# Kernel tuning notes

Measured on AMD Instinct MI355X. Metric: run time of the kernel, lower is better.

The kernel has to match this reference:

```python
import jax, jax.numpy as jnp
import numpy as np


def setup_inputs() -> dict:
    key = jax.random.key(0)
    ks = jax.random.split(key, 6)
    B, C, H, W = 8, 512, 64, 64
    s = 1.0 / np.sqrt(C)
    return {
        "x": jax.random.normal(ks[0], (B, C, H, W), dtype=jnp.float32),
        "w_phi": jax.random.normal(ks[1], (C, C), dtype=jnp.float32) * s,
        "w_theta": jax.random.normal(ks[2], (C, C), dtype=jnp.float32) * s,
        "w_g": jax.random.normal(ks[3], (C, C), dtype=jnp.float32) * s,
        "w_mask": jax.random.normal(ks[4], (C, C), dtype=jnp.float32) * s,
        "gamma": jax.random.normal(ks[5], (1,), dtype=jnp.float32) * 0.1,
    }


def reference(x, w_phi, w_theta, w_g, w_mask, gamma):
    b, c, h, w = x.shape
    n = h * w
    xf = x.reshape(b, c, n)  # flatten spatial: [b, c, n]
    # 1x1 convs (bias=False) are channel-mixing GEMMs
    phi = jnp.einsum("oc,bcn->bon", w_phi, xf)    # [b, c, n]
    theta = jnp.einsum("oc,bcn->bon", w_theta, xf)  # [b, c, n]
    g = jnp.einsum("oc,bcn->bon", w_g, xf)        # [b, c, n]
    # channel-channel attention (unscaled), softmax over last dim
    attn = jax.nn.softmax(jnp.einsum("bcn,bdn->bcd", phi, theta), axis=-1)  # [b, c, c]
    y = jnp.einsum("bcd,bdn->bcn", attn, g)  # [b, c, n]
    # faithful to torch: permute(0,2,1).contiguous().view(b, c, h, w)
    y = jnp.transpose(y, (0, 2, 1)).reshape(b, c, h, w)
    mask = jnp.einsum("oc,bchw->bohw", w_mask, y)
    return mask * gamma[0] + x
```

## Files before the change

### kernel.cpp

```cpp
#include <hip/hip_runtime.h>
#include <hip/hip_bf16.h>

constexpr int BATCH = 8;
constexpr int C = 512;
constexpr int HW = 4096;
constexpr long CN = (long)C * HW;
constexpr long CC = (long)C * C;

typedef __attribute__((ext_vector_type(8))) short short8;
typedef __attribute__((ext_vector_type(4))) short bf16x4;
typedef __attribute__((ext_vector_type(4))) float f32x4;

__device__ __forceinline__ void gload16(const void* g, void* l) {
  __builtin_amdgcn_global_load_lds(
      (const __attribute__((address_space(1))) void*)g,
      (__attribute__((address_space(3))) void*)l, 16, 0, 0);
}

__device__ __forceinline__ void hilo(float v, __hip_bfloat16& h, __hip_bfloat16& l) {
  h = __float2bfloat16(v);
  l = __float2bfloat16(v - __bfloat162float(h));
}
__device__ __forceinline__ short bfs(float v) {
  __hip_bfloat16 h = __float2bfloat16(v);
  return *(short*)&h;
}

__device__ __forceinline__ int cidx32(int r, int ch) {
  return ((r >> 1) * 8 + ((((r & 1) << 2) | ch) ^ ((r >> 1) & 7))) * 8;
}
__device__ __forceinline__ void sdec32(int s, int& r, int& ch) {
  int R = s >> 3, q = s & 7, v = q ^ (R & 7);
  r = (R << 1) | (v >> 2);
  ch = v & 3;
}

#define WAIT_VM(n) asm volatile("s_waitcnt vmcnt(" #n ")" ::: "memory")

__global__ __launch_bounds__(256) void convx_k(
    const float* __restrict__ x, __hip_bfloat16* __restrict__ xhi,
    __hip_bfloat16* __restrict__ xt) {
  const int b = blockIdx.z;
  const int n0 = blockIdx.x * 64, c0 = blockIdx.y * 64;
  const float* xb = x + (long)b * CN;
  __shared__ short t[64 * 65];
  const int tid = threadIdx.x;
#pragma unroll
  for (int it = 0; it < 2; ++it) {
    int slot = it * 256 + tid;
    int r = slot >> 3, cc = (slot & 7) * 8;
    const float* src = xb + (long)(c0 + r) * HW + n0 + cc;
    f32x4 v0 = *(const f32x4*)src, v1 = *(const f32x4*)(src + 4);
    short8 hh;
#pragma unroll
    for (int e = 0; e < 4; ++e) {
      hh[e] = bfs(v0[e]);
      hh[4 + e] = bfs(v1[e]);
    }
    long idx = (long)b * CN + (long)(c0 + r) * HW + n0 + cc;
    *(short8*)((short*)xhi + idx) = hh;
#pragma unroll
    for (int e = 0; e < 8; ++e) t[r * 65 + cc + e] = hh[e];
  }
  __syncthreads();
#pragma unroll
  for (int it = 0; it < 2; ++it) {
    int slot = it * 256 + tid;
    int r = slot >> 3, cc = (slot & 7) * 8;
    short8 o;
#pragma unroll
    for (int e = 0; e < 8; ++e) o[e] = t[(cc + e) * 65 + r];
    *(short8*)((short*)xt + (long)b * CN + (long)(n0 + r) * C + c0 + cc) = o;
  }
}

__global__ __launch_bounds__(256) void wprep_k(
    const float* __restrict__ wphi, const float* __restrict__ wtheta,
    const float* __restrict__ wg, const float* __restrict__ wmask,
    __hip_bfloat16* __restrict__ wph, __hip_bfloat16* __restrict__ wpl,
    __hip_bfloat16* __restrict__ wth, __hip_bfloat16* __restrict__ wtl,
    __hip_bfloat16* __restrict__ wgT, __hip_bfloat16* __restrict__ wm16) {
  const int z = blockIdx.z;
  const int r0 = blockIdx.y * 64, c0 = blockIdx.x * 64;
  const int tid = threadIdx.x;
  if (z == 2) {
    __shared__ __hip_bfloat16 t[64][65];
#pragma unroll
    for (int i = 0; i < 16; ++i) {
      int e = i * 256 + tid;
      int r = e >> 6, c = e & 63;
      t[r][c] = __float2bfloat16(wg[(long)(r0 + r) * C + c0 + c]);
    }
    __syncthreads();
#pragma unroll
    for (int i = 0; i < 16; ++i) {
      int e = i * 256 + tid;
      int r = e >> 6, c = e & 63;
      wgT[(long)(c0 + r) * C + r0 + c] = t[c][r];
    }
  } else {
#pragma unroll
    for (int i = 0; i < 16; ++i) {
      int e = i * 256 + tid;
      int r = e >> 6, c = e & 63;
      long idx = (long)(r0 + r) * C + c0 + c;
      if (z == 0) {
        __hip_bfloat16 h, l;
        hilo(wphi[idx], h, l);
        wph[idx] = h; wpl[idx] = l;
      } else if (z == 1) {
        __hip_bfloat16 h, l;
        hilo(wtheta[idx], h, l);
        wth[idx] = h; wtl[idx] = l;
      } else {
        wm16[idx] = __float2bfloat16(wmask[idx]);
      }
    }
  }
}

__global__ __launch_bounds__(256) void gram_k(
    const __hip_bfloat16* __restrict__ xhi, float* __restrict__ gpart) {
  const int f = blockIdx.x + 10 * (blockIdx.y + 4 * blockIdx.z);
  const int b = f & 7;
  const int rdec = f >> 3;
  const int ks = rdec / 10;
  const int tile = rdec % 10;
  int i = 0, rem0 = tile;
  while (rem0 >= 4 - i) { rem0 -= 4 - i; ++i; }
  const int j = i + rem0;
  const int m0 = i * 128, n0 = j * 128;

  const short* X = (const short*)(xhi + (long)b * CN);
  __shared__ short lds[4 * 8192];
  const int tid = threadIdx.x, w = tid >> 6, lane = tid & 63;

  f32x4 acc[4][4] = {};
  const int wr = (w >> 1) * 64, wc = (w & 1) * 64;
  const int kbeg = ks * 1024;
  constexpr int NST = 32;

  auto STAGE = [&](int buf, int k0) {
#pragma unroll
    for (int it = 0; it < 4; ++it) {
      int s = (w & 1) * 256 + it * 64 + lane;
      int r, ch;
      sdec32(s, r, ch);
      int gr = (w < 2) ? (m0 + r) : (n0 + r);
      gload16(X + (long)gr * HW + k0 + ch * 8, lds + (buf * 8192 + (w >> 1) * 4096 + s * 8));
    }
  };

  const int chf = lane >> 4, rl = lane & 15;
  int aoff[4], boff[4];
#pragma unroll
  for (int mi = 0; mi < 4; ++mi) aoff[mi] = cidx32(wr + mi * 16 + rl, chf);
#pragma unroll
  for (int ni = 0; ni < 4; ++ni) boff[ni] = 4096 + cidx32(wc + ni * 16 + rl, chf);

  STAGE(0, kbeg);
  STAGE(1, kbeg + 32);
  STAGE(2, kbeg + 64);

#pragma unroll
  for (int t = 0; t < NST; ++t) {
    if (t + 3 < NST) STAGE((t + 3) & 3, kbeg + (t + 3) * 32);
    const int rm = NST - 1 - t;
    if (rm >= 3) WAIT_VM(12);
    else if (rm == 2) WAIT_VM(8);
    else if (rm == 1) WAIT_VM(4);
    else WAIT_VM(0);
    __builtin_amdgcn_s_barrier();
    const short* lb = lds + (t & 3) * 8192;
    short8 af[4], bfr[4];
#pragma unroll
    for (int mi = 0; mi < 4; ++mi) af[mi] = *(const short8*)(lb + aoff[mi]);
#pragma unroll
    for (int ni = 0; ni < 4; ++ni) bfr[ni] = *(const short8*)(lb + boff[ni]);
#pragma unroll
    for (int mi = 0; mi < 4; ++mi)
#pragma unroll
      for (int ni = 0; ni < 4; ++ni)
        acc[mi][ni] = __builtin_amdgcn_mfma_f32_16x16x32_bf16(af[mi], bfr[ni], acc[mi][ni], 0, 0, 0);
    __builtin_amdgcn_s_barrier();
  }

  float* P = gpart + ((((long)b * 10 + tile) * 4 + ks) << 14);
#pragma unroll
  for (int mi = 0; mi < 4; ++mi)
#pragma unroll
    for (int ni = 0; ni < 4; ++ni)
#pragma unroll
      for (int rr = 0; rr < 4; ++rr) {
        int row = wr + mi * 16 + (lane >> 4) * 4 + rr;
        int col = wc + ni * 16 + (lane & 15);
        P[row * 128 + col] = acc[mi][ni][rr];
      }
}

__global__ __launch_bounds__(256) void gred_k(
    const float* __restrict__ gpart, __hip_bfloat16* __restrict__ gh,
    __hip_bfloat16* __restrict__ gl) {
  const int id = blockIdx.x;
  const int b = id & 7;
  const int t2 = id >> 3;
  const int tile = t2 % 10;
  const int half = t2 / 10;
  int i = 0, rem = tile;
  while (rem >= 4 - i) { rem -= 4 - i; ++i; }
  const int j = i + rem;
  const int m0 = i * 128, n0 = j * 128;
  const float* P = gpart + (((long)b * 10 + tile) << 16) + half * 8192;
  __shared__ float T[128][65];
  const int tid = threadIdx.x;
  const long dbase = (long)b * CC;

#pragma unroll
  for (int q = 0; q < 8; ++q) {
    int e = q * 1024 + tid * 4;
    int r = e >> 7, c = e & 127;
    f32x4 s = {};
#pragma unroll
    for (int ks = 0; ks < 4; ++ks) s += *(const f32x4*)(P + (ks << 14) + e);
    bf16x4 hh, ll;
#pragma unroll
    for (int u = 0; u < 4; ++u) {
      __hip_bfloat16 h, l;
      hilo(s[u], h, l);
      hh[u] = *(short*)&h;
      ll[u] = *(short*)&l;
      T[c + u][r] = s[u];
    }
    long idx = dbase + (long)(m0 + half * 64 + r) * 512 + n0 + c;
    *(bf16x4*)((short*)gh + idx) = hh;
    *(bf16x4*)((short*)gl + idx) = ll;
  }
  if (i != j) {
    __syncthreads();
#pragma unroll
    for (int q = 0; q < 8; ++q) {
      int e = q * 1024 + tid * 4;
      int rp = e >> 6, cp = e & 63;
      bf16x4 hh, ll;
#pragma unroll
      for (int u = 0; u < 4; ++u) {
        __hip_bfloat16 h, l;
        hilo(T[rp][cp + u], h, l);
        hh[u] = *(short*)&h;
        ll[u] = *(short*)&l;
      }
      long idx = dbase + (long)(n0 + rp) * 512 + m0 + half * 64 + cp;
      *(bf16x4*)((short*)gh + idx) = hh;
      *(bf16x4*)((short*)gl + idx) = ll;
    }
  }
}

template <int AH, int BH, int EPI>
__global__ __launch_bounds__(256) void nt_small(
    const __hip_bfloat16* __restrict__ Ah_, const __hip_bfloat16* __restrict__ Al_,
    const __hip_bfloat16* __restrict__ Bh_, const __hip_bfloat16* __restrict__ Bl_,
    long aStr, long bStr, void* __restrict__ out1, void* __restrict__ out2) {
  const int id = blockIdx.x;
  const int b = id & 7;
  const int rest = id >> 3;
  const int m0 = (rest >> 3) * 64, n0 = (rest & 7) * 64;
  const short* Ahp = (const short*)(Ah_ + (long)b * aStr);
  const short* Alp = AH ? (const short*)(Al_ + (long)b * aStr) : nullptr;
  const short* Bhp = (const short*)(Bh_ + (long)b * bStr);
  const short* Blp = BH ? (const short*)(Bl_ + (long)b * bStr) : nullptr;
  constexpr int PAN = (AH && BH) ? 4 : 2;
  __shared__ short lds[2 * PAN * 4096];
  const int tid = threadIdx.x, w = tid >> 6, lane = tid & 63;

  f32x4 acc[2][2] = {};
  const int wr = (w >> 1) * 32, wc = (w & 1) * 32;

  auto STAGE = [&](int buf, int k0) {
    short* lb = lds + buf * PAN * 4096;
    if constexpr (AH && BH) {
      const short* src = (w == 0) ? Ahp : (w == 1) ? Alp : (w == 2) ? Bhp : Blp;
      const int rowbase = (w & 2) ? n0 : m0;
      short* lt = lb + w * 4096;
#pragma unroll
      for (int it = 0; it < 8; ++it) {
        int slot = it * 64 + lane;
        int r = slot >> 3, p = slot & 7, c = p ^ (r & 7);
        gload16(src + (long)(rowbase + r) * 512 + k0 + c * 8, lt + slot * 8);
      }
    } else {
      const short* src = (w < 2) ? Ahp : Bhp;
      const int rowbase = (w < 2) ? m0 : n0;
      short* lt = lb + (w >> 1) * 4096;
#pragma unroll
      for (int it = 0; it < 4; ++it) {
        int slot = (w & 1) * 256 + it * 64 + lane;
        int r = slot >> 3, p = slot & 7, c = p ^ (r & 7);
        gload16(src + (long)(rowbase + r) * 512 + k0 + c * 8, lt + slot * 8);
      }
    }
  };

  STAGE(0, 0);
  asm volatile("s_waitcnt vmcnt(0)" ::: "memory");
  __builtin_amdgcn_s_barrier();

  for (int t = 0; t < 8; ++t) {
    if (t < 7) STAGE((t + 1) & 1, (t + 1) * 64);
    const short* lb = lds + (t & 1) * PAN * 4096;
#pragma unroll
    for (int kh = 0; kh < 2; ++kh) {
      short8 ah[2], al[2], bh[2], bl[2];
      const int ch = kh * 4 + (lane >> 4);
#pragma unroll
      for (int mi = 0; mi < 2; ++mi) {
        int r = wr + mi * 16 + (lane & 15);
        int off = (r * 8 + (ch ^ (r & 7))) * 8;
        ah[mi] = *(const short8*)(lb + off);
        if constexpr (AH) al[mi] = *(const short8*)(lb + 4096 + off);
      }
#pragma unroll
      for (int ni = 0; ni < 2; ++ni) {
        int r = wc + ni * 16 + (lane & 15);
        int off = (r * 8 + (ch ^ (r & 7))) * 8;
        bh[ni] = *(const short8*)(lb + ((AH && BH) ? 8192 : 4096) + off);
        if constexpr (BH) bl[ni] = *(const short8*)(lb + 12288 + off);
      }
#pragma unroll
      for (int mi = 0; mi < 2; ++mi)
#pragma unroll
        for (int ni = 0; ni < 2; ++ni) {
          acc[mi][ni] = __builtin_amdgcn_mfma_f32_16x16x32_bf16(ah[mi], bh[ni], acc[mi][ni], 0, 0, 0);
          if constexpr (BH)
            acc[mi][ni] = __builtin_amdgcn_mfma_f32_16x16x32_bf16(ah[mi], bl[ni], acc[mi][ni], 0, 0, 0);
          if constexpr (AH)
            acc[mi][ni] = __builtin_amdgcn_mfma_f32_16x16x32_bf16(al[mi], bh[ni], acc[mi][ni], 0, 0, 0);
        }
    }
    asm volatile("s_waitcnt vmcnt(0)" ::: "memory");
    __builtin_amdgcn_s_barrier();
  }

#pragma unroll
  for (int mi = 0; mi < 2; ++mi)
#pragma unroll
    for (int ni = 0; ni < 2; ++ni)
#pragma unroll
      for (int rr = 0; rr < 4; ++rr) {
        int row = m0 + wr + mi * 16 + (lane >> 4) * 4 + rr;
        int col = n0 + wc + ni * 16 + (lane & 15);
        long idx = (long)b * CC + (long)row * 512 + col;
        float v = acc[mi][ni][rr];
        if constexpr (EPI == 0) {
          __hip_bfloat16 h, l;
          hilo(v, h, l);
          ((__hip_bfloat16*)out1)[idx] = h;
          ((__hip_bfloat16*)out2)[idx] = l;
        } else if constexpr (EPI == 1) {
          ((float*)out1)[idx] = v;
        } else {
          ((__hip_bfloat16*)out1)[idx] = __float2bfloat16(v);
        }
      }
}

__global__ __launch_bounds__(256) void softmax_k(const float* __restrict__ a,
                                                 __hip_bfloat16* __restrict__ o) {
  const int id = blockIdx.x;
  const int b = id & 7, rg = id >> 3;
  const int w = threadIdx.x >> 6, lane = threadIdx.x & 63;
  const long row = (long)b * 512 + rg * 4 + w;
  const float* rp = a + row * 512 + lane * 8;
  f32x4 v0 = *(const f32x4*)rp, v1 = *(const f32x4*)(rp + 4);
  float mx = fmaxf(fmaxf(fmaxf(v0[0], v0[1]), fmaxf(v0[2], v0[3])),
                   fmaxf(fmaxf(v1[0], v1[1]), fmaxf(v1[2], v1[3])));
#pragma unroll
  for (int s = 1; s < 64; s <<= 1) mx = fmaxf(mx, __shfl_xor(mx, s));
  float e[8];
#pragma unroll
  for (int k = 0; k < 4; ++k) {
    e[k] = expf(v0[k] - mx);
    e[4 + k] = expf(v1[k] - mx);
  }
  float sum = ((e[0] + e[1]) + (e[2] + e[3])) + ((e[4] + e[5]) + (e[6] + e[7]));
#pragma unroll
  for (int s = 1; s < 64; s <<= 1) sum += __shfl_xor(sum, s);
  const float inv = 1.0f / sum;
  short8 o8;
#pragma unroll
  for (int k = 0; k < 8; ++k) o8[k] = bfs(e[k] * inv);
  *(short8*)((short*)o + row * 512 + lane * 8) = o8;
}

template <int MODE>
__global__ __launch_bounds__(256) void big_k(
    const __hip_bfloat16* __restrict__ Aw, const __hip_bfloat16* __restrict__ Bm,
    void* __restrict__ Cout, const float* __restrict__ x,
    const float* __restrict__ gammaPtr, long aStride) {
  const int b = blockIdx.z;
  const int lin = ((blockIdx.x & 7) << 4) | (blockIdx.x >> 3);
  const int m0 = (lin & 3) * 128;
  const int n0 = (lin >> 2) * 128;
  const short* A = (const short*)(Aw + (long)b * aStride);
  const short* B = (const short*)(Bm + (long)b * CN);
  __shared__ short lds[4 * 8192];
  const int tid = threadIdx.x, w = tid >> 6, lane = tid & 63;

  f32x4 acc[4][4] = {};
  const int wr = (w >> 1) * 64, wc = (w & 1) * 64;
  constexpr int NST = 16;

  auto STAGE = [&](int buf, int k0) {
    short* lb = lds + buf * 8192;
#pragma unroll
    for (int it = 0; it < 4; ++it) {
      int s = (w & 1) * 256 + it * 64 + lane;
      int r, ch;
      sdec32(s, r, ch);
      if (w < 2) {
        gload16(A + (long)(m0 + r) * 512 + k0 + ch * 8, lb + s * 8);
      } else {
        int gr = (MODE == 0) ? (n0 + (r & 15) * 8 + (r >> 4)) : (n0 + r);
        gload16(B + (long)gr * 512 + k0 + ch * 8, lb + 4096 + s * 8);
      }
    }
  };

  const int chf = lane >> 4, rl = lane & 15;
  int aoff[4], boff[4];
#pragma unroll
  for (int mi = 0; mi < 4; ++mi) aoff[mi] = cidx32(wr + mi * 16 + rl, chf);
#pragma unroll
  for (int ni = 0; ni < 4; ++ni) boff[ni] = 4096 + cidx32(wc + ni * 16 + rl, chf);

  STAGE(0, 0);
  STAGE(1, 32);
  STAGE(2, 64);

#pragma unroll
  for (int t = 0; t < NST; ++t) {
    if (t + 3 < NST) STAGE((t + 3) & 3, (t + 3) * 32);
    const int rm = NST - 1 - t;
    if (rm >= 3) WAIT_VM(12);
    else if (rm == 2) WAIT_VM(8);
    else if (rm == 1) WAIT_VM(4);
    else WAIT_VM(0);
    __builtin_amdgcn_s_barrier();
    const short* lb = lds + (t & 3) * 8192;
    short8 af[4], bfr[4];
#pragma unroll
    for (int mi = 0; mi < 4; ++mi) af[mi] = *(const short8*)(lb + aoff[mi]);
#pragma unroll
    for (int ni = 0; ni < 4; ++ni) bfr[ni] = *(const short8*)(lb + boff[ni]);
#pragma unroll
    for (int mi = 0; mi < 4; ++mi)
#pragma unroll
      for (int ni = 0; ni < 4; ++ni)
        acc[mi][ni] = __builtin_amdgcn_mfma_f32_16x16x32_bf16(af[mi], bfr[ni], acc[mi][ni], 0, 0, 0);
    __builtin_amdgcn_s_barrier();
  }

  if (MODE == 0) {
    __hip_bfloat16* yv = (__hip_bfloat16*)Cout + (long)b * CN;
    const int u = lane & 15;
#pragma unroll
    for (int mi = 0; mi < 4; ++mi)
#pragma unroll
      for (int ni = 0; ni < 4; ++ni) {
        int t = (wc >> 4) + ni;
        long base = ((long)(t * 512 + m0 + wr + mi * 16 + (lane >> 4) * 4)) * 512 +
                    (n0 >> 3) + u;
#pragma unroll
        for (int r = 0; r < 4; ++r)
          yv[base + (long)r * 512] = __float2bfloat16(acc[mi][ni][r]);
      }
  } else {
    float* outp = (float*)Cout + (long)b * CN;
    const float* xb = x + (long)b * CN;
    const float g0 = gammaPtr[0];
#pragma unroll
    for (int mi = 0; mi < 4; ++mi)
#pragma unroll
      for (int ni = 0; ni < 4; ++ni)
#pragma unroll
        for (int r = 0; r < 4; ++r) {
          long idx = (long)(m0 + wr + mi * 16 + (lane >> 4) * 4 + r) * HW +
                     n0 + wc + ni * 16 + (lane & 15);
          outp[idx] = g0 * acc[mi][ni][r] + xb[idx];
        }
  }
}

extern "C" void kernel_launch(void* const* d_in, const int* in_sizes, int n_in,
                              void* d_out, int out_size, void* d_ws, size_t ws_size,
                              hipStream_t stream) {
  const float* x       = (const float*)d_in[0];
  const float* w_phi   = (const float*)d_in[1];
  const float* w_theta = (const float*)d_in[2];
  const float* w_g     = (const float*)d_in[3];
  const float* w_mask  = (const float*)d_in[4];
  const float* gamma   = (const float*)d_in[5];
  float* out = (float*)d_out;

  __hip_bfloat16* xhi = (__hip_bfloat16*)d_ws;
  __hip_bfloat16* xt  = xhi + BATCH * CN;
  __hip_bfloat16* gh  = xt + BATCH * CN;
  __hip_bfloat16* gl  = gh + BATCH * CC;
  __hip_bfloat16* t1h = gl + BATCH * CC;
  __hip_bfloat16* t1l = t1h + BATCH * CC;
  __hip_bfloat16* wph = t1l + BATCH * CC;
  __hip_bfloat16* wpl = wph + CC;
  __hip_bfloat16* wth = wpl + CC;
  __hip_bfloat16* wtl = wth + CC;
  __hip_bfloat16* wgT = wtl + CC;
  __hip_bfloat16* wm16 = wgT + CC;
  float* gpart = (float*)(wm16 + CC);
  float* logits           = (float*)gh;
  __hip_bfloat16* attn16  = t1h;
  __hip_bfloat16* mb16    = t1l;
  __hip_bfloat16* yvT     = xhi;

  convx_k<<<dim3(64, 8, BATCH), 256, 0, stream>>>(x, xhi, xt);
  wprep_k<<<dim3(8, 8, 4), 256, 0, stream>>>(w_phi, w_theta, w_g, w_mask,
                                             wph, wpl, wth, wtl, wgT, wm16);
  gram_k<<<dim3(10, 4, BATCH), 256, 0, stream>>>(xhi, gpart);
  gred_k<<<dim3(160, 1, 1), 256, 0, stream>>>(gpart, gh, gl);
  nt_small<1, 1, 0><<<dim3(512, 1, 1), 256, 0, stream>>>(
      wph, wpl, gh, gl, 0, CC, t1h, t1l);
  nt_small<1, 1, 1><<<dim3(512, 1, 1), 256, 0, stream>>>(
      t1h, t1l, wth, wtl, CC, 0, logits, nullptr);
  softmax_k<<<dim3(1024, 1, 1), dim3(256), 0, stream>>>(logits, attn16);
  nt_small<0, 0, 2><<<dim3(512, 1, 1), 256, 0, stream>>>(
      attn16, nullptr, wgT, nullptr, CC, 0, mb16, nullptr);
  big_k<0><<<dim3(128, 1, BATCH), 256, 0, stream>>>(mb16, xt, yvT, nullptr, nullptr, CC);
  big_k<1><<<dim3(128, 1, BATCH), 256, 0, stream>>>(wm16, yvT, out, x, gamma, 0);
}
```

Measured before the change: 255.6 us.

## Deepen nt_small to 4-stage pipeline and prefetch residual x during GEMM loop

The small channel-attention GEMM kernel moves from a double-buffered BK=64 loop with full vmcnt(0) drains to the 4-buffer BK=32 pipeline used by big_k, with partial waitcnts and precomputed swizzled LDS offsets. The final mask GEMM now loads the residual x tile into registers across the K loop, so the epilogue no longer stalls on global reads. The cost is more registers (64 floats of x per thread) in the big kernel, which may lower occupancy. The tuned vmcnt thresholds also have to match the exact number of outstanding loads.

```diff
diff --git a/kernel.cpp b/kernel.cpp
--- a/kernel.cpp
+++ b/kernel.cpp
@@ -270,74 +270,89 @@
   const short* Bhp = (const short*)(Bh_ + (long)b * bStr);
   const short* Blp = BH ? (const short*)(Bl_ + (long)b * bStr) : nullptr;
   constexpr int PAN = (AH && BH) ? 4 : 2;
-  __shared__ short lds[2 * PAN * 4096];
+  constexpr int BUFS = PAN * 2048;
+  __shared__ short lds[4 * BUFS];
   const int tid = threadIdx.x, w = tid >> 6, lane = tid & 63;
 
   f32x4 acc[2][2] = {};
   const int wr = (w >> 1) * 32, wc = (w & 1) * 32;
+  constexpr int NST = 16;
 
   auto STAGE = [&](int buf, int k0) {
-    short* lb = lds + buf * PAN * 4096;
     if constexpr (AH && BH) {
       const short* src = (w == 0) ? Ahp : (w == 1) ? Alp : (w == 2) ? Bhp : Blp;
       const int rowbase = (w & 2) ? n0 : m0;
-      short* lt = lb + w * 4096;
-#pragma unroll
-      for (int it = 0; it < 8; ++it) {
-        int slot = it * 64 + lane;
-        int r = slot >> 3, p = slot & 7, c = p ^ (r & 7);
-        gload16(src + (long)(rowbase + r) * 512 + k0 + c * 8, lt + slot * 8);
+#pragma unroll
+      for (int it = 0; it < 4; ++it) {
+        int s = it * 64 + lane;
+        int r, ch;
+        sdec32(s, r, ch);
+        gload16(src + (long)(rowbase + r) * 512 + k0 + ch * 8,
+                lds + ((buf * PAN + w) * 2048 + s * 8));
       }
     } else {
       const short* src = (w < 2) ? Ahp : Bhp;
       const int rowbase = (w < 2) ? m0 : n0;
-      short* lt = lb + (w >> 1) * 4096;
-#pragma unroll
-      for (int it = 0; it < 4; ++it) {
-        int slot = (w & 1) * 256 + it * 64 + lane;
-        int r = slot >> 3, p = slot & 7, c = p ^ (r & 7);
-        gload16(src + (long)(rowbase + r) * 512 + k0 + c * 8, lt + slot * 8);
+#pragma unroll
+      for (int it = 0; it < 2; ++it) {
+        int s = (w & 1) * 128 + it * 64 + lane;
+        int r, ch;
+        sdec32(s, r, ch);
+        gload16(src + (long)(rowbase + r) * 512 + k0 + ch * 8,
+                lds + ((buf * PAN + (w >> 1)) * 2048 + s * 8));
       }
     }
   };
 
+  const int chf = lane >> 4, rl = lane & 15;
+  int aoff[2], boff[2];
+#pragma unroll
+  for (int mi = 0; mi < 2; ++mi) aoff[mi] = cidx32(wr + mi * 16 + rl, chf);
+#pragma unroll
+  for (int ni = 0; ni < 2; ++ni) boff[ni] = cidx32(wc + ni * 16 + rl, chf);
+
   STAGE(0, 0);
-  asm volatile("s_waitcnt vmcnt(0)" ::: "memory");
-  __builtin_amdgcn_s_barrier();
-
-  for (int t = 0; t < 8; ++t) {
-    if (t < 7) STAGE((t + 1) & 1, (t + 1) * 64);
-    const short* lb = lds + (t & 1) * PAN * 4096;
-#pragma unroll
-    for (int kh = 0; kh < 2; ++kh) {
-      short8 ah[2], al[2], bh[2], bl[2];
-      const int ch = kh * 4 + (lane >> 4);
-#pragma unroll
-      for (int mi = 0; mi < 2; ++mi) {
-        int r = wr + mi * 16 + (lane & 15);
-        int off = (r * 8 + (ch ^ (r & 7))) * 8;
-        ah[mi] = *(const short8*)(lb + off);
-        if constexpr (AH) al[mi] = *(const short8*)(lb + 4096 + off);
-      }
+  STAGE(1, 32);
+  STAGE(2, 64);
+
+#pragma unroll
+  for (int t = 0; t < NST; ++t) {
+    if (t + 3 < NST) STAGE((t + 3) & 3, (t + 3) * 32);
+    const int rm = NST - 1 - t;
+    if constexpr (PAN == 4) {
+      if (rm >= 3) WAIT_VM(12);
+      else if (rm == 2) WAIT_VM(8);
+      else if (rm == 1) WAIT_VM(4);
+      else WAIT_VM(0);
+    } else {
+      if (rm >= 3) WAIT_VM(6);
+      else if (rm == 2) WAIT_VM(4);
+      else if (rm == 1) WAIT_VM(2);
+      else WAIT_VM(0);
+    }
+    __builtin_amdgcn_s_barrier();
+    const short* lb = lds + (t & 3) * BUFS;
+    short8 ah[2], al[2], bh[2], bl[2];
+#pragma unroll
+    for (int mi = 0; mi < 2; ++mi) {
+      ah[mi] = *(const short8*)(lb + aoff[mi]);
+      if constexpr (AH) al[mi] = *(const short8*)(lb + 2048 + aoff[mi]);
+    }
+#pragma unroll
+    for (int ni = 0; ni < 2; ++ni) {
+      bh[ni] = *(const short8*)(lb + ((AH && BH) ? 4096 : 2048) + boff[ni]);
+      if constexpr (BH) bl[ni] = *(const short8*)(lb + 6144 + boff[ni]);
+    }
+#pragma unroll
+    for (int mi = 0; mi < 2; ++mi)
 #pragma unroll
       for (int ni = 0; ni < 2; ++ni) {
-        int r = wc + ni * 16 + (lane & 15);
-        int off = (r * 8 + (ch ^ (r & 7))) * 8;
-        bh[ni] = *(const short8*)(lb + ((AH && BH) ? 8192 : 4096) + off);
-        if constexpr (BH) bl[ni] = *(const short8*)(lb + 12288 + off);
-      }
-#pragma unroll
-      for (int mi = 0; mi < 2; ++mi)
-#pragma unroll
-        for (int ni = 0; ni < 2; ++ni) {
-          acc[mi][ni] = __builtin_amdgcn_mfma_f32_16x16x32_bf16(ah[mi], bh[ni], acc[mi][ni], 0, 0, 0);
-          if constexpr (BH)
-            acc[mi][ni] = __builtin_amdgcn_mfma_f32_16x16x32_bf16(ah[mi], bl[ni], acc[mi][ni], 0, 0, 0);
-          if constexpr (AH)
-            acc[mi][ni] = __builtin_amdgcn_mfma_f32_16x16x32_bf16(al[mi], bh[ni], acc[mi][ni], 0, 0, 0);
-        }
-    }
-    asm volatile("s_waitcnt vmcnt(0)" ::: "memory");
+        acc[mi][ni] = __builtin_amdgcn_mfma_f32_16x16x32_bf16(ah[mi], bh[ni], acc[mi][ni], 0, 0, 0);
+        if constexpr (BH)
+          acc[mi][ni] = __builtin_amdgcn_mfma_f32_16x16x32_bf16(ah[mi], bl[ni], acc[mi][ni], 0, 0, 0);
+        if constexpr (AH)
+          acc[mi][ni] = __builtin_amdgcn_mfma_f32_16x16x32_bf16(al[mi], bh[ni], acc[mi][ni], 0, 0, 0);
+      }
     __builtin_amdgcn_s_barrier();
   }
 
@@ -410,6 +425,9 @@
   const int wr = (w >> 1) * 64, wc = (w & 1) * 64;
   constexpr int NST = 16;
 
+  const float* xb = (MODE == 1) ? x + (long)b * CN : nullptr;
+  float xv[16][4];
+
   auto STAGE = [&](int buf, int k0) {
     short* lb = lds + buf * 8192;
 #pragma unroll
@@ -440,11 +458,28 @@
 #pragma unroll
   for (int t = 0; t < NST; ++t) {
     if (t + 3 < NST) STAGE((t + 3) & 3, (t + 3) * 32);
+    if constexpr (MODE == 1) {
+      const int mi = t >> 2, ni = t & 3;
+      const long base = (long)(m0 + wr + mi * 16 + chf * 4) * HW +
+                        n0 + wc + ni * 16 + rl;
+#pragma unroll
+      for (int r = 0; r < 4; ++r) xv[t][r] = xb[base + (long)r * HW];
+    }
     const int rm = NST - 1 - t;
-    if (rm >= 3) WAIT_VM(12);
-    else if (rm == 2) WAIT_VM(8);
-    else if (rm == 1) WAIT_VM(4);
-    else WAIT_VM(0);
+    if constexpr (MODE == 1) {
+      if (t == 0) WAIT_VM(16);
+      else if (t == 1) WAIT_VM(20);
+      else if (t == 2) WAIT_VM(24);
+      else if (t <= 12) WAIT_VM(28);
+      else if (t == 13) WAIT_VM(24);
+      else if (t == 14) WAIT_VM(20);
+      else WAIT_VM(16);
+    } else {
+      if (rm >= 3) WAIT_VM(12);
+      else if (rm == 2) WAIT_VM(8);
+      else if (rm == 1) WAIT_VM(4);
+      else WAIT_VM(0);
+    }
     __builtin_amdgcn_s_barrier();
     const short* lb = lds + (t & 3) * 8192;
     short8 af[4], bfr[4];
@@ -475,8 +510,8 @@
           yv[base + (long)r * 512] = __float2bfloat16(acc[mi][ni][r]);
       }
   } else {
+    WAIT_VM(0);
     float* outp = (float*)Cout + (long)b * CN;
-    const float* xb = x + (long)b * CN;
     const float g0 = gammaPtr[0];
 #pragma unroll
     for (int mi = 0; mi < 4; ++mi)
@@ -484,9 +519,9 @@
       for (int ni = 0; ni < 4; ++ni)
 #pragma unroll
         for (int r = 0; r < 4; ++r) {
-          long idx = (long)(m0 + wr + mi * 16 + (lane >> 4) * 4 + r) * HW +
-                     n0 + wc + ni * 16 + (lane & 15);
-          outp[idx] = g0 * acc[mi][ni][r] + xb[idx];
+          long idx = (long)(m0 + wr + mi * 16 + chf * 4 + r) * HW +
+                     n0 + wc + ni * 16 + rl;
+          outp[idx] = g0 * acc[mi][ni][r] + xv[mi * 4 + ni][r];
         }
   }
 }
```

Measured after the change: 262.4 us. +2.7%, slower.
